# Performance work log

Hardware: AMD Instinct MI355X
Metric: run time of the kernel (lower is better)

## Reference

```python
import jax, jax.numpy as jnp
import numpy as np

INPUT_DIM = 1024
HIDDEN = 1024
MASKED = INPUT_DIM // 2  # even indices are the conditioning half
BATCH = 65536


def setup_inputs() -> dict:
    key = jax.random.key(0)
    ks = jax.random.split(key, 7)
    s1 = 1.0 / np.sqrt(MASKED)
    s2 = 1.0 / np.sqrt(HIDDEN)
    x = jax.random.normal(ks[0], (BATCH, INPUT_DIM), dtype=jnp.float32)
    W1 = jax.random.uniform(ks[1], (MASKED, HIDDEN), jnp.float32, -s1, s1)
    b1 = jax.random.uniform(ks[2], (HIDDEN,), jnp.float32, -s1, s1)
    W2 = jax.random.uniform(ks[3], (HIDDEN, HIDDEN), jnp.float32, -s2, s2)
    b2 = jax.random.uniform(ks[4], (HIDDEN,), jnp.float32, -s2, s2)
    W3 = jax.random.uniform(ks[5], (HIDDEN, INPUT_DIM - MASKED), jnp.float32, -s2, s2)
    b3 = jax.random.uniform(ks[6], (INPUT_DIM - MASKED,), jnp.float32, -s2, s2)
    return {"x": x, "W1": W1, "b1": b1, "W2": W2, "b2": b2, "W3": W3, "b3": b3}


def reference(x, W1, b1, W2, b2, W3, b3):
    # mask_type='even': mask[::2]=1 -> even indices conditioning, odd indices translated
    masked = x[:, 0::2]  # [B, MASKED], gather of conditioning half
    h = jax.nn.relu(masked @ W1 + b1)
    h = jax.nn.relu(h @ W2 + b2)
    translation = h @ W3 + b3  # [B, INPUT_DIM - MASKED]
    # scatter-add translation into odd positions
    y = x.at[:, 1::2].add(translation)
    return y
```

## Files before the change

### kernel.cpp

```cpp
#include <hip/hip_runtime.h>
#include <stdint.h>

#define BATCH  65536
#define IN_DIM 1024
#define MASKED 512
#define HIDDEN 1024

typedef unsigned short u16;
typedef __bf16 bf16x8 __attribute__((ext_vector_type(8)));
typedef float  f32x4  __attribute__((ext_vector_type(4)));

typedef __attribute__((address_space(1))) void gvoid;
typedef __attribute__((address_space(3))) void lvoid;

__device__ __forceinline__ u16 f32_to_bf16(float f) {
    union { float f; uint32_t u; } v; v.f = f;
    uint32_t r = v.u + 0x7FFFu + ((v.u >> 16) & 1u);
    return (u16)(r >> 16);
}

__global__ void prep_xm(const float* __restrict__ x, u16* __restrict__ xm) {
    int idx = blockIdx.x * blockDim.x + threadIdx.x;
    const float4* xv = reinterpret_cast<const float4*>(x);
    float4 v0 = xv[idx * 2];
    float4 v1 = xv[idx * 2 + 1];
    ushort4 o;
    o.x = f32_to_bf16(v0.x);
    o.y = f32_to_bf16(v0.z);
    o.z = f32_to_bf16(v1.x);
    o.w = f32_to_bf16(v1.z);
    reinterpret_cast<ushort4*>(xm)[idx] = o;
}

__global__ void wconv(const float* __restrict__ W, u16* __restrict__ Wt,
                      int K, int N) {
    __shared__ float t[32][33];
    const int nbk = K / 32;
    const int bk = blockIdx.x % nbk;
    const int bn = blockIdx.x / nbk;
    const int tx = threadIdx.x & 31;
    const int ty = threadIdx.x >> 5;
    const int k0 = bk * 32, n0 = bn * 32;
    #pragma unroll
    for (int i = 0; i < 4; ++i)
        t[ty + i * 8][tx] = W[(int64_t)(k0 + ty + i * 8) * N + n0 + tx];
    __syncthreads();
    #pragma unroll
    for (int i = 0; i < 4; ++i)
        Wt[(int64_t)(n0 + ty + i * 8) * K + k0 + tx] = f32_to_bf16(t[tx][ty + i * 8]);
}

template<int K, int N, int MODE>
__global__ __launch_bounds__(256, 4)
void gemm_bt(const u16* __restrict__ A, const u16* __restrict__ Bt,
             const float* __restrict__ bias,
             u16* __restrict__ Cb,
             const float* __restrict__ X,
             float* __restrict__ Y) {
    constexpr int BK = 64;
    __shared__ u16 As[128 * BK];
    __shared__ u16 Bs[128 * BK];

    const int tid  = threadIdx.x;
    const int lane = tid & 63;
    const int w    = tid >> 6;
    const int wr   = w >> 1;
    const int wc   = w & 1;

    const int nwg = gridDim.x;
    const int cpx = nwg >> 3;
    const int bid = (blockIdx.x & 7) * cpx + (blockIdx.x >> 3);

    constexpr int nbn = N / 128;
    const int bm = bid / nbn;
    const int bn = bid % nbn;
    const int m0 = bm * 128;
    const int n0 = bn * 128;

    f32x4 acc[4][4];
    #pragma unroll
    for (int i = 0; i < 4; ++i)
        #pragma unroll
        for (int j = 0; j < 4; ++j)
            acc[i][j] = f32x4{0.f, 0.f, 0.f, 0.f};

    const int srow = lane >> 3;
    const int scol = (lane & 7) * 8;
    const u16* aptr = A  + (int64_t)(m0 + w * 32 + srow) * K + scol;
    const u16* bptr = Bt + (int64_t)(n0 + w * 32 + srow) * K + scol;

    for (int kt = 0; kt < K / BK; ++kt) {
        __syncthreads();
        const int koff = kt * BK;
        #pragma unroll
        for (int c = 0; c < 4; ++c) {
            __builtin_amdgcn_global_load_lds(
                (gvoid*)(aptr + koff + c * 8 * K),
                (lvoid*)(&As[(w * 32 + c * 8) * BK]), 16, 0, 0);
            __builtin_amdgcn_global_load_lds(
                (gvoid*)(bptr + koff + c * 8 * K),
                (lvoid*)(&Bs[(w * 32 + c * 8) * BK]), 16, 0, 0);
        }
        __syncthreads();

        #pragma unroll
        for (int kk = 0; kk < 2; ++kk) {
            bf16x8 a[4], b[4];
            #pragma unroll
            for (int i = 0; i < 4; ++i)
                a[i] = *reinterpret_cast<const bf16x8*>(
                    &As[(wr * 64 + i * 16 + (lane & 15)) * BK + kk * 32 + (lane >> 4) * 8]);
            #pragma unroll
            for (int j = 0; j < 4; ++j)
                b[j] = *reinterpret_cast<const bf16x8*>(
                    &Bs[(wc * 64 + j * 16 + (lane & 15)) * BK + kk * 32 + (lane >> 4) * 8]);
            #pragma unroll
            for (int i = 0; i < 4; ++i)
                #pragma unroll
                for (int j = 0; j < 4; ++j)
                    acc[i][j] = __builtin_amdgcn_mfma_f32_16x16x32_bf16(
                        a[i], b[j], acc[i][j], 0, 0, 0);
        }
    }

    const int cl = lane & 15;
    const int rg = (lane >> 4) * 4;
    #pragma unroll
    for (int j = 0; j < 4; ++j) {
        const int n  = n0 + wc * 64 + j * 16 + cl;
        const float bv = bias[n];
        #pragma unroll
        for (int i = 0; i < 4; ++i) {
            #pragma unroll
            for (int r = 0; r < 4; ++r) {
                const int m = m0 + wr * 64 + i * 16 + rg + r;
                float v = acc[i][j][r] + bv;
                if (MODE == 0) {
                    v = v > 0.f ? v : 0.f;
                    Cb[(int64_t)m * N + n] = f32_to_bf16(v);
                } else {
                    const int64_t p = (int64_t)m * IN_DIM + 2 * n;
                    float2 xv = *reinterpret_cast<const float2*>(&X[p]);
                    float2 o;
                    o.x = xv.x;
                    o.y = xv.y + v;
                    *reinterpret_cast<float2*>(&Y[p]) = o;
                }
            }
        }
    }
}

extern "C" void kernel_launch(void* const* d_in, const int* in_sizes, int n_in,
                              void* d_out, int out_size, void* d_ws, size_t ws_size,
                              hipStream_t stream) {
    const float* x  = (const float*)d_in[0];
    const float* W1 = (const float*)d_in[1];
    const float* b1 = (const float*)d_in[2];
    const float* W2 = (const float*)d_in[3];
    const float* b2 = (const float*)d_in[4];
    const float* W3 = (const float*)d_in[5];
    const float* b3 = (const float*)d_in[6];
    float* y = (float*)d_out;

    char* ws = (char*)d_ws;
    u16* h1  = (u16*)(ws);
    u16* h2  = (u16*)(ws + 134217728);
    u16* xm  = (u16*)(ws + 134217728);
    u16* W1t = (u16*)(ws + 268435456);
    u16* W2t = (u16*)(ws + 268435456 + 1048576);
    u16* W3t = (u16*)(ws + 268435456 + 1048576 + 2097152);

    prep_xm<<<BATCH * IN_DIM / 8 / 256, 256, 0, stream>>>(x, xm);

    wconv<<<(MASKED / 32) * (HIDDEN / 32), 256, 0, stream>>>(W1, W1t, MASKED, HIDDEN);
    wconv<<<(HIDDEN / 32) * (HIDDEN / 32), 256, 0, stream>>>(W2, W2t, HIDDEN, HIDDEN);
    wconv<<<(HIDDEN / 32) * ((IN_DIM - MASKED) / 32), 256, 0, stream>>>(W3, W3t, HIDDEN, IN_DIM - MASKED);

    gemm_bt<MASKED, HIDDEN, 0><<<(BATCH / 128) * (HIDDEN / 128), 256, 0, stream>>>(
        xm, W1t, b1, h1, nullptr, nullptr);
    gemm_bt<HIDDEN, HIDDEN, 0><<<(BATCH / 128) * (HIDDEN / 128), 256, 0, stream>>>(
        h1, W2t, b2, h2, nullptr, nullptr);
    gemm_bt<HIDDEN, IN_DIM - MASKED, 1><<<(BATCH / 128) * ((IN_DIM - MASKED) / 128), 256, 0, stream>>>(
        h2, W3t, b3, nullptr, x, y);
}
```

Baseline: 469.8 us.

## Rewrite GEMMs as 256x256 tiles with 4-stage async LDS pipeline

Replaces the 128x128, 256-thread GEMM with a 256x256, 512-thread tile using a 4-deep ring of LDS buffers filled by direct global-to-LDS loads issued three k-steps ahead. Each k-step is split into two halves so the next stage's loads interleave with MFMA work, with explicit vmcnt waits, barriers and s_setprio around the MFMA blocks. The aim is to hide global-load latency and raise data reuse per tile. In exchange it uses more LDS and registers, which lowers occupancy, and it depends on hand-placed waitcnt and barrier ordering being correct.

```diff
diff --git a/kernel.cpp b/kernel.cpp
--- a/kernel.cpp
+++ b/kernel.cpp
@@ -12,6 +12,10 @@
 
 typedef __attribute__((address_space(1))) void gvoid;
 typedef __attribute__((address_space(3))) void lvoid;
+
+#define WAITV(N) asm volatile("s_waitcnt vmcnt(" #N ")" ::: "memory")
+#define WAITL0() asm volatile("s_waitcnt lgkmcnt(0)" ::: "memory")
+#define FENCE()  asm volatile("" ::: "memory")
 
 __device__ __forceinline__ u16 f32_to_bf16(float f) {
     union { float f; uint32_t u; } v; v.f = f;
@@ -51,90 +55,120 @@
 }
 
 template<int K, int N, int MODE>
-__global__ __launch_bounds__(256, 4)
-void gemm_bt(const u16* __restrict__ A, const u16* __restrict__ Bt,
+__global__ __launch_bounds__(512, 2)
+void gemm256(const u16* __restrict__ A, const u16* __restrict__ Bt,
              const float* __restrict__ bias,
              u16* __restrict__ Cb,
              const float* __restrict__ X,
              float* __restrict__ Y) {
-    constexpr int BK = 64;
-    __shared__ u16 As[128 * BK];
-    __shared__ u16 Bs[128 * BK];
+    constexpr int BK = 32;
+    constexpr int NT = K / BK;
+    __shared__ __align__(16) u16 As[4][256 * BK];
+    __shared__ __align__(16) u16 Bs[4][256 * BK];
 
     const int tid  = threadIdx.x;
     const int lane = tid & 63;
     const int w    = tid >> 6;
-    const int wr   = w >> 1;
-    const int wc   = w & 1;
+    const int wm   = w >> 2;
+    const int wn   = w & 3;
 
     const int nwg = gridDim.x;
     const int cpx = nwg >> 3;
     const int bid = (blockIdx.x & 7) * cpx + (blockIdx.x >> 3);
-
-    constexpr int nbn = N / 128;
-    const int bm = bid / nbn;
-    const int bn = bid % nbn;
-    const int m0 = bm * 128;
-    const int n0 = bn * 128;
-
-    f32x4 acc[4][4];
-    #pragma unroll
-    for (int i = 0; i < 4; ++i)
+    constexpr int nbn = N / 256;
+    const int m0 = (bid / nbn) * 256;
+    const int n0 = (bid % nbn) * 256;
+
+    const int srow = w * 16 + (lane >> 2);
+    const int sg   = (lane & 3) * 8;
+    const u16* aS = A  + (int64_t)(m0 + srow) * K + sg;
+    const u16* bS = Bt + (int64_t)(n0 + srow) * K + sg;
+    const int lOff = w * 512;
+
+#define STG_A1(kt) __builtin_amdgcn_global_load_lds((gvoid*)(aS + (kt)*BK),          (lvoid*)(&As[(kt)&3][lOff]),        16, 0, 0)
+#define STG_A2(kt) __builtin_amdgcn_global_load_lds((gvoid*)(aS + 128*K + (kt)*BK),  (lvoid*)(&As[(kt)&3][4096 + lOff]), 16, 0, 0)
+#define STG_B1(kt) __builtin_amdgcn_global_load_lds((gvoid*)(bS + (kt)*BK),          (lvoid*)(&Bs[(kt)&3][lOff]),        16, 0, 0)
+#define STG_B2(kt) __builtin_amdgcn_global_load_lds((gvoid*)(bS + 128*K + (kt)*BK),  (lvoid*)(&Bs[(kt)&3][4096 + lOff]), 16, 0, 0)
+
+    f32x4 acc[8][4];
+    #pragma unroll
+    for (int i = 0; i < 8; ++i)
         #pragma unroll
         for (int j = 0; j < 4; ++j)
             acc[i][j] = f32x4{0.f, 0.f, 0.f, 0.f};
 
-    const int srow = lane >> 3;
-    const int scol = (lane & 7) * 8;
-    const u16* aptr = A  + (int64_t)(m0 + w * 32 + srow) * K + scol;
-    const u16* bptr = Bt + (int64_t)(n0 + w * 32 + srow) * K + scol;
-
-    for (int kt = 0; kt < K / BK; ++kt) {
-        __syncthreads();
-        const int koff = kt * BK;
-        #pragma unroll
-        for (int c = 0; c < 4; ++c) {
-            __builtin_amdgcn_global_load_lds(
-                (gvoid*)(aptr + koff + c * 8 * K),
-                (lvoid*)(&As[(w * 32 + c * 8) * BK]), 16, 0, 0);
-            __builtin_amdgcn_global_load_lds(
-                (gvoid*)(bptr + koff + c * 8 * K),
-                (lvoid*)(&Bs[(w * 32 + c * 8) * BK]), 16, 0, 0);
-        }
-        __syncthreads();
-
-        #pragma unroll
-        for (int kk = 0; kk < 2; ++kk) {
-            bf16x8 a[4], b[4];
+    STG_A1(0); STG_A2(0); STG_B1(0); STG_B2(0);
+    STG_A1(1); STG_A2(1); STG_B1(1); STG_B2(1);
+    STG_A1(2); STG_A2(2); STG_B1(2); STG_B2(2);
+    WAITV(8);
+    __builtin_amdgcn_s_barrier();
+    FENCE();
+
+    const int arow = wm * 128 + (lane & 15);
+    const int brow = wn * 64  + (lane & 15);
+    const int kcol = (lane >> 4) * 8;
+
+    for (int kt = 0; kt < NT; ++kt) {
+        const int s = kt & 3;
+        const u16* Asl = As[s];
+        const u16* Bsl = Bs[s];
+        bf16x8 a[4], b[4];
+
+        #pragma unroll
+        for (int mf = 0; mf < 4; ++mf)
+            a[mf] = *reinterpret_cast<const bf16x8*>(&Asl[(arow + mf * 16) * BK + kcol]);
+        #pragma unroll
+        for (int nf = 0; nf < 4; ++nf)
+            b[nf] = *reinterpret_cast<const bf16x8*>(&Bsl[(brow + nf * 16) * BK + kcol]);
+        if (kt + 3 < NT) { STG_A1(kt + 3); STG_B1(kt + 3); }
+        __builtin_amdgcn_s_setprio(1);
+        #pragma unroll
+        for (int mf = 0; mf < 4; ++mf)
             #pragma unroll
-            for (int i = 0; i < 4; ++i)
-                a[i] = *reinterpret_cast<const bf16x8*>(
-                    &As[(wr * 64 + i * 16 + (lane & 15)) * BK + kk * 32 + (lane >> 4) * 8]);
+            for (int nf = 0; nf < 4; ++nf)
+                acc[mf][nf] = __builtin_amdgcn_mfma_f32_16x16x32_bf16(
+                    a[mf], b[nf], acc[mf][nf], 0, 0, 0);
+        __builtin_amdgcn_s_setprio(0);
+        __builtin_amdgcn_s_barrier();
+        FENCE();
+
+        bf16x8 a2[4];
+        #pragma unroll
+        for (int mf = 0; mf < 4; ++mf)
+            a2[mf] = *reinterpret_cast<const bf16x8*>(&Asl[(arow + 64 + mf * 16) * BK + kcol]);
+        if (kt + 3 < NT) { STG_A2(kt + 3); STG_B2(kt + 3); }
+        __builtin_amdgcn_s_setprio(1);
+        #pragma unroll
+        for (int mf = 0; mf < 4; ++mf)
             #pragma unroll
-            for (int j = 0; j < 4; ++j)
-                b[j] = *reinterpret_cast<const bf16x8*>(
-                    &Bs[(wc * 64 + j * 16 + (lane & 15)) * BK + kk * 32 + (lane >> 4) * 8]);
-            #pragma unroll
-            for (int i = 0; i < 4; ++i)
-                #pragma unroll
-                for (int j = 0; j < 4; ++j)
-                    acc[i][j] = __builtin_amdgcn_mfma_f32_16x16x32_bf16(
-                        a[i], b[j], acc[i][j], 0, 0, 0);
+            for (int nf = 0; nf < 4; ++nf)
+                acc[mf + 4][nf] = __builtin_amdgcn_mfma_f32_16x16x32_bf16(
+                    a2[mf], b[nf], acc[mf + 4][nf], 0, 0, 0);
+        __builtin_amdgcn_s_setprio(0);
+
+        WAITL0();
+        __builtin_amdgcn_sched_barrier(0);
+        if (kt < NT - 3)       { WAITV(8); }
+        else if (kt == NT - 3) { WAITV(4); }
+        else if (kt == NT - 2) { WAITV(0); }
+        if (kt < NT - 1) {
+            __builtin_amdgcn_s_barrier();
+            FENCE();
         }
     }
 
     const int cl = lane & 15;
     const int rg = (lane >> 4) * 4;
     #pragma unroll
-    for (int j = 0; j < 4; ++j) {
-        const int n  = n0 + wc * 64 + j * 16 + cl;
+    for (int nf = 0; nf < 4; ++nf) {
+        const int n  = n0 + wn * 64 + nf * 16 + cl;
         const float bv = bias[n];
         #pragma unroll
-        for (int i = 0; i < 4; ++i) {
+        for (int mf = 0; mf < 8; ++mf) {
             #pragma unroll
             for (int r = 0; r < 4; ++r) {
-                const int m = m0 + wr * 64 + i * 16 + rg + r;
-                float v = acc[i][j][r] + bv;
+                const int m = m0 + wm * 128 + mf * 16 + rg + r;
+                float v = acc[mf][nf][r] + bv;
                 if (MODE == 0) {
                     v = v > 0.f ? v : 0.f;
                     Cb[(int64_t)m * N + n] = f32_to_bf16(v);
@@ -149,6 +183,10 @@
             }
         }
     }
+#undef STG_A1
+#undef STG_A2
+#undef STG_B1
+#undef STG_B2
 }
 
 extern "C" void kernel_launch(void* const* d_in, const int* in_sizes, int n_in,
@@ -177,10 +215,10 @@
     wconv<<<(HIDDEN / 32) * (HIDDEN / 32), 256, 0, stream>>>(W2, W2t, HIDDEN, HIDDEN);
     wconv<<<(HIDDEN / 32) * ((IN_DIM - MASKED) / 32), 256, 0, stream>>>(W3, W3t, HIDDEN, IN_DIM - MASKED);
 
-    gemm_bt<MASKED, HIDDEN, 0><<<(BATCH / 128) * (HIDDEN / 128), 256, 0, stream>>>(
+    gemm256<MASKED, HIDDEN, 0><<<(BATCH / 256) * (HIDDEN / 256), 512, 0, stream>>>(
         xm, W1t, b1, h1, nullptr, nullptr);
-    gemm_bt<HIDDEN, HIDDEN, 0><<<(BATCH / 128) * (HIDDEN / 128), 256, 0, stream>>>(
+    gemm256<HIDDEN, HIDDEN, 0><<<(BATCH / 256) * (HIDDEN / 256), 512, 0, stream>>>(
         h1, W2t, b2, h2, nullptr, nullptr);
-    gemm_bt<HIDDEN, IN_DIM - MASKED, 1><<<(BATCH / 128) * ((IN_DIM - MASKED) / 128), 256, 0, stream>>>(
+    gemm256<HIDDEN, IN_DIM - MASKED, 1><<<(BATCH / 256) * ((IN_DIM - MASKED) / 256), 512, 0, stream>>>(
         h2, W3t, b3, nullptr, x, y);
 }
```

Result: slower. 525.7 us (+11.9%).
